# Kernel tuning notes

Measured on AMD Instinct MI355X. Metric: run time of the kernel, lower is better.

## Reference

```python
import jax, jax.numpy as jnp
import numpy as np

N_NODES = 50000
EPS = 1e-16


def seg_softmax(att, seg, n):
    # att: [E, H], softmax over edges sharing the same destination (seg)
    m = jax.ops.segment_max(att, seg, num_segments=n)
    m = jnp.where(jnp.isfinite(m), m, 0.0)
    e = jnp.exp(att - m[seg])
    s = jax.ops.segment_sum(e, seg, num_segments=n)
    return e / (s[seg] + EPS)


def gat_layer(x, W, b, a_l, a_r, row, col, n, nhead, out_feats, alpha, act):
    h = (x @ W).reshape(-1, nhead, out_feats)           # [N, H, F]
    h = jnp.nan_to_num(h)
    h_l = jnp.sum(a_l * h, axis=-1)                     # [N, H]
    h_r = jnp.sum(a_r * h, axis=-1)                     # [N, H]
    e = h_l[row] + h_r[col]                             # [E, H]
    e = jax.nn.leaky_relu(e, negative_slope=alpha)
    att = seg_softmax(e, row, n)                        # softmax per destination node
    # sparse multi-head aggregation: out[i] = sum_{e: row[e]=i} att[e] * h[col[e]]
    msg = att[:, :, None] * h[col]                      # [E, H, F]
    out = jax.ops.segment_sum(msg, row, num_segments=n) # [N, H, F]
    out = out.reshape(n, nhead * out_feats) + b
    if act:
        out = jax.nn.relu(out)
    return out


def setup_inputs() -> dict:
    key = jax.random.key(0)
    ks = jax.random.split(key, 10)
    N, E = N_NODES, 800000
    x = jax.random.normal(ks[0], (N, 256), dtype=jnp.float32)
    row = jax.random.randint(ks[1], (E,), 0, N)
    col = jax.random.randint(ks[2], (E,), 0, N)
    g = 1.414  # xavier-like scale handled via normal * small std
    W1 = jax.random.normal(ks[3], (256, 128), dtype=jnp.float32) * (g / np.sqrt(256 + 128))
    b1 = jnp.zeros((128,), dtype=jnp.float32)
    al1 = jax.random.normal(ks[4], (1, 4, 32), dtype=jnp.float32) * 0.1
    ar1 = jax.random.normal(ks[5], (1, 4, 32), dtype=jnp.float32) * 0.1
    W2 = jax.random.normal(ks[6], (128, 64), dtype=jnp.float32) * (g / np.sqrt(128 + 64))
    b2 = jnp.zeros((64,), dtype=jnp.float32)
    al2 = jax.random.normal(ks[7], (1, 1, 64), dtype=jnp.float32) * 0.1
    ar2 = jax.random.normal(ks[8], (1, 1, 64), dtype=jnp.float32) * 0.1
    return {"x": x, "row": row, "col": col, "W1": W1, "b1": b1, "al1": al1,
            "ar1": ar1, "W2": W2, "b2": b2, "al2": al2, "ar2": ar2}


def reference(x, row, col, W1, b1, al1, ar1, W2, b2, al2, ar2):
    n = N_NODES
    h = gat_layer(x, W1, b1, al1, ar1, row, col, n, nhead=4, out_feats=32, alpha=0.2, act=True)
    out = gat_layer(h, W2, b2, al2, ar2, row, col, n, nhead=1, out_feats=64, alpha=0.2, act=False)
    return out
```

## Files before the change

kernel.cpp:

```cpp
#include <hip/hip_runtime.h>
#include <hip/hip_bf16.h>
#include <hip/hip_fp16.h>
#include <math.h>

#define ALPHA 0.2f
#define LOG2E 1.44269504088896f
#define CAP 8192

typedef _Float16 half8 __attribute__((ext_vector_type(8)));
typedef float f32x4 __attribute__((ext_vector_type(4)));
typedef float f32x2 __attribute__((ext_vector_type(2)));

__global__ __launch_bounds__(256) void setup_kernel(
    int* __restrict__ gcursor,
    const float* __restrict__ W1, _Float16* __restrict__ W1t,
    const float* __restrict__ W2, _Float16* __restrict__ W2t) {
    const int blk = blockIdx.x, tid = threadIdx.x;
    if (blk == 0) {
        gcursor[tid] = 0;
    } else if (blk <= 128) {
        int i = (blk - 1) * 256 + tid;
        int k = i >> 7, c = i & 127;
        W1t[c * 256 + k] = (_Float16)W1[i];
    } else {
        int j = (blk - 129) * 256 + tid;
        int k = j >> 6, c = j & 63;
        W2t[c * 128 + k] = (_Float16)W2[j];
    }
}


__device__ __forceinline__ void part_body(char* smem, int blk,
                                          const int* __restrict__ row,
                                          const int* __restrict__ col,
                                          int* __restrict__ gcursor,
                                          unsigned* __restrict__ tmp, int E) {
    int* h = (int*)smem;
    int* rsv = h + 256;
    const int tid = threadIdx.x;
    const int base = blk * 4096;
    h[tid] = 0;
    __syncthreads();
#pragma unroll
    for (int k = 0; k < 16; ++k) {
        int i = base + k * 256 + tid;
        if (i < E) atomicAdd(&h[row[i] >> 8], 1);
    }
    __syncthreads();
    if (h[tid]) rsv[tid] = atomicAdd(&gcursor[tid], h[tid]);
    __syncthreads();
    h[tid] = 0;
    __syncthreads();
#pragma unroll
    for (int k = 0; k < 16; ++k) {
        int i = base + k * 256 + tid;
        if (i < E) {
            int r = row[i];
            int b = r >> 8;
            int loc = atomicAdd(&h[b], 1);
            tmp[(size_t)b * CAP + rsv[b] + loc] = ((unsigned)r << 16) | (unsigned)col[i];
        }
    }
}

__device__ __forceinline__ void bucket_body(char* smem, int k,
                                            const unsigned* __restrict__ tmp,
                                            const int* __restrict__ gcursor,
                                            unsigned* __restrict__ startcnt,
                                            unsigned short* __restrict__ csr_col, int N) {
    int* h = (int*)smem;
    int* rs = h + 256;
    int* wtot = rs + 256;
    const int tid = threadIdx.x;
    const int lane = tid & 63, wid = tid >> 6;
    const int base = k * CAP;
    const int count = gcursor[k];
    h[tid] = 0;
    __syncthreads();
    for (int p = tid; p < count; p += 256) atomicAdd(&h[(tmp[base + p] >> 16) & 255], 1);
    __syncthreads();
    int v = h[tid];
    int sc = v;
#pragma unroll
    for (int d = 1; d < 64; d <<= 1) {
        int u = __shfl_up(sc, d);
        if (lane >= d) sc += u;
    }
    if (lane == 63) wtot[wid] = sc;
    __syncthreads();
    int add = 0;
    for (int w = 0; w < wid; ++w) add += wtot[w];
    rs[tid] = sc - v + add + base;
    __syncthreads();
    int gr = k * 256 + tid;
    if (gr < N) startcnt[gr] = ((unsigned)rs[tid] << 11) | (unsigned)v;
    h[tid] = 0;
    __syncthreads();
    for (int p = tid; p < count; p += 256) {
        unsigned t = tmp[base + p];
        int rl = (t >> 16) & 255;
        int loc = atomicAdd(&h[rl], 1);
        csr_col[rs[rl] + loc] = (unsigned short)(t & 0xFFFF);
    }
}

__device__ __forceinline__ void gemm1_body(char* smem, int tile,
                                           const float* __restrict__ x,
                                           const _Float16* __restrict__ Wt,
                                           const float* __restrict__ al,
                                           const float* __restrict__ ar,
                                           unsigned char* __restrict__ h8,
                                           float* __restrict__ hl,
                                           float* __restrict__ hr, int N) {
    const int tid = threadIdx.x;
    const int lane = tid & 63, wc = tid >> 6;
    const int row0 = tile * 32;
    const int col0 = wc * 32;

#pragma unroll
    for (int it = 0; it < 8; ++it) {
        int i = it * 256 + tid;
        int r = i >> 6, c4 = i & 63;
        int gr = row0 + r;
        float4 v = {0.f, 0.f, 0.f, 0.f};
        if (gr < N) v = *(const float4*)(x + (size_t)gr * 256 + c4 * 4);
        union { _Float16 p[4]; uint2 u; } pk;
        pk.p[0] = (_Float16)v.x; pk.p[1] = (_Float16)v.y;
        pk.p[2] = (_Float16)v.z; pk.p[3] = (_Float16)v.w;
        int byte = r * 512 + c4 * 8;
        byte ^= (r & 7) << 4;
        *reinterpret_cast<uint2*>(smem + byte) = pk.u;
    }

    const _Float16* wbase = Wt + (size_t)(col0 + (lane & 15)) * 256 + (lane >> 4) * 8;

    __syncthreads();

    f32x4 acc[2][2] = {};
    half8 bf0[2], bf1[2], af0[2], af1[2];

    auto loadB = [&](int s, half8* dst) {
        dst[0] = *(const half8*)(wbase + s * 32);
        dst[1] = *(const half8*)(wbase + 16 * 256 + s * 32);
    };
    auto loadA = [&](int s, half8* dst) {
#pragma unroll
        for (int m = 0; m < 2; ++m) {
            int r = m * 16 + (lane & 15);
            int byte = r * 512 + s * 64 + (lane >> 4) * 16;
            byte ^= (r & 7) << 4;
            dst[m] = *reinterpret_cast<const half8*>(smem + byte);
        }
    };
    auto domfma = [&](half8* a, half8* bvec) {
#pragma unroll
        for (int m = 0; m < 2; ++m)
#pragma unroll
            for (int n = 0; n < 2; ++n)
                acc[m][n] = __builtin_amdgcn_mfma_f32_16x16x32_f16(
                    a[m], bvec[n], acc[m][n], 0, 0, 0);
    };

    loadB(0, bf0); loadA(0, af0);
#pragma unroll
    for (int s = 0; s < 8; s += 2) {
        if (s + 1 < 8) { loadB(s + 1, bf1); loadA(s + 1, af1); }
        domfma(af0, bf0);
        if (s + 2 < 8) { loadB(s + 2, bf0); loadA(s + 2, af0); }
        if (s + 1 < 8) domfma(af1, bf1);
    }

#pragma unroll
    for (int m = 0; m < 2; ++m) {
        int grow_base = row0 + m * 16 + (lane >> 4) * 4;
#pragma unroll
        for (int n = 0; n < 2; ++n) {
            int gcol = col0 + n * 16 + (lane & 15);
#pragma unroll
            for (int reg = 0; reg < 4; ++reg) {
                int grow = grow_base + reg;
                if (grow < N) {
                    unsigned pkv = __builtin_amdgcn_cvt_pk_fp8_f32(
                        acc[m][n][reg], acc[m][n][reg], 0, false);
                    h8[(size_t)grow * 128 + gcol] = (unsigned char)(pkv & 0xFF);
                }
            }
        }
    }

    const float al0 = al[col0 + (lane & 15)],      ar0 = ar[col0 + (lane & 15)];
    const float al1 = al[col0 + 16 + (lane & 15)], ar1 = ar[col0 + 16 + (lane & 15)];
#pragma unroll
    for (int m = 0; m < 2; ++m) {
#pragma unroll
        for (int reg = 0; reg < 4; ++reg) {
            float l = al0 * acc[m][0][reg] + al1 * acc[m][1][reg];
            float r = ar0 * acc[m][0][reg] + ar1 * acc[m][1][reg];
#pragma unroll
            for (int msk = 1; msk < 16; msk <<= 1) {
                l += __shfl_xor(l, msk);
                r += __shfl_xor(r, msk);
            }
            int grow = row0 + m * 16 + (lane >> 4) * 4 + reg;
            if ((lane & 15) == 0 && grow < N) {
                hl[grow * 4 + wc] = l * LOG2E;
                hr[grow * 4 + wc] = r * LOG2E;
            }
        }
    }
}

__global__ __launch_bounds__(256) void ka_kernel(
    const int* __restrict__ row, const int* __restrict__ col,
    int* __restrict__ gcursor, unsigned* __restrict__ tmp, int E, int eblocks,
    const float* __restrict__ x, const _Float16* __restrict__ W1t,
    const float* __restrict__ al, const float* __restrict__ ar,
    unsigned char* __restrict__ h8, float* __restrict__ hl, float* __restrict__ hr,
    int N, int tile0)
{
    __shared__ __align__(16) char smem[16384];
    if (blockIdx.x < (unsigned)eblocks)
        part_body(smem, blockIdx.x, row, col, gcursor, tmp, E);
    else
        gemm1_body(smem, tile0 + blockIdx.x - eblocks, x, W1t, al, ar, h8, hl, hr, N);
}

__global__ __launch_bounds__(256) void kb_kernel(
    const unsigned* __restrict__ tmp, const int* __restrict__ gcursor,
    unsigned* __restrict__ startcnt, unsigned short* __restrict__ csr_col,
    int nbuck,
    const float* __restrict__ x, const _Float16* __restrict__ W1t,
    const float* __restrict__ al, const float* __restrict__ ar,
    unsigned char* __restrict__ h8, float* __restrict__ hl, float* __restrict__ hr,
    int N, int tile0)
{
    __shared__ __align__(16) char smem[16384];
    if (blockIdx.x < (unsigned)nbuck)
        bucket_body(smem, blockIdx.x, tmp, gcursor, startcnt, csr_col, N);
    else
        gemm1_body(smem, tile0 + blockIdx.x - nbuck, x, W1t, al, ar, h8, hl, hr, N);
}

__global__ __launch_bounds__(256) void agg1g2_kernel(
    const unsigned* __restrict__ startcnt, const unsigned short* __restrict__ csr_col,
    const float* __restrict__ hls, const float* __restrict__ hrs,
    const unsigned char* __restrict__ h8, const float* __restrict__ b,
    const _Float16* __restrict__ W2t,
    const float* __restrict__ al, const float* __restrict__ ar,
    _Float16* __restrict__ h2, float* __restrict__ hl2, float* __restrict__ hr2, int N)
{
    __shared__ __align__(16) char rows[16 * 256];
    __shared__ float plds[16][4], prds[16][4];
    const int tid = threadIdx.x;
    const int lane = tid & 63, wid = tid >> 6;
    const int node0 = blockIdx.x * 16;
    const int q = lane >> 4;
    const int fl = lane & 15;
    const int head = fl >> 2;

    float bp[8];
#pragma unroll
    for (int k = 0; k < 8; ++k) bp[k] = b[8 * fl + k];

    for (int j = 0; j < 4; ++j) {
        const int i = node0 + wid * 4 + j;
        const int r = wid * 4 + j;
        float acc[8] = {};
        float den = 0.f;
        bool live = i < N;
        if (live) {
            const unsigned pk = startcnt[i];
            const int s = (int)(pk >> 11), e = s + (int)(pk & 2047);
            const float hlv = hls[i * 4 + head];

            int p0 = s + q;
            bool v0 = p0 < e;
            int cc0 = v0 ? (int)csr_col[p0] : 0;
            float hr0 = hrs[cc0 * 4 + head];
            uint2 g0 = *(const uint2*)(h8 + (size_t)cc0 * 128 + 8 * fl);

#pragma unroll 2
            for (int pb = s; pb < e; pb += 4) {
                int p1 = pb + 4 + q;
                bool v1 = p1 < e;
                int cc1 = v1 ? (int)csr_col[p1] : 0;
                float hr1v = hrs[cc1 * 4 + head];
                uint2 g1 = *(const uint2*)(h8 + (size_t)cc1 * 128 + 8 * fl);

                float sc = hlv + hr0;
                sc = sc > 0.f ? sc : ALPHA * sc;
                float w = exp2f(sc);
                w = v0 ? w : 0.f;
                den += w;
                f32x2 p01 = __builtin_amdgcn_cvt_pk_f32_fp8(g0.x, false);
                f32x2 p23 = __builtin_amdgcn_cvt_pk_f32_fp8(g0.x, true);
                f32x2 p45 = __builtin_amdgcn_cvt_pk_f32_fp8(g0.y, false);
                f32x2 p67 = __builtin_amdgcn_cvt_pk_f32_fp8(g0.y, true);
                acc[0] = fmaf(w, p01[0], acc[0]);
                acc[1] = fmaf(w, p01[1], acc[1]);
                acc[2] = fmaf(w, p23[0], acc[2]);
                acc[3] = fmaf(w, p23[1], acc[3]);
                acc[4] = fmaf(w, p45[0], acc[4]);
                acc[5] = fmaf(w, p45[1], acc[5]);
                acc[6] = fmaf(w, p67[0], acc[6]);
                acc[7] = fmaf(w, p67[1], acc[7]);

                v0 = v1; cc0 = cc1; hr0 = hr1v; g0 = g1;
            }

            den += __shfl_xor(den, 16); den += __shfl_xor(den, 32);
#pragma unroll
            for (int k = 0; k < 8; ++k) {
                acc[k] += __shfl_xor(acc[k], 16);
                acc[k] += __shfl_xor(acc[k], 32);
            }
        }
        if (lane < 16) {
            union { uint4 u; _Float16 q8[8]; } ov;
            if (live) {
                float rcp = 1.f / (den + 1e-16f);
#pragma unroll
                for (int k = 0; k < 8; ++k) {
                    float o = acc[k] * rcp + bp[k];
                    o = o > 0.f ? o : 0.f;
                    ov.q8[k] = (_Float16)o;
                }
            } else {
                ov.u = make_uint4(0, 0, 0, 0);
            }
            int byte = r * 256 + fl * 16;
            byte ^= (r & 7) << 4;
            *reinterpret_cast<uint4*>(rows + byte) = ov.u;
        }
    }
    __syncthreads();

    const int wc = wid;
    const int col0 = wc * 16;
    const _Float16* wbase = W2t + (size_t)(col0 + (lane & 15)) * 128 + (lane >> 4) * 8;

    f32x4 acc2 = {};
    half8 bf0, bf1, af0, af1;

    auto loadA = [&](int s, half8& dst) {
        int r = lane & 15;
        int byte = r * 256 + s * 64 + (lane >> 4) * 16;
        byte ^= (r & 7) << 4;
        dst = *reinterpret_cast<const half8*>(rows + byte);
    };

    bf0 = *(const half8*)(wbase); loadA(0, af0);
#pragma unroll
    for (int s = 0; s < 4; s += 2) {
        if (s + 1 < 4) { bf1 = *(const half8*)(wbase + (s + 1) * 32); loadA(s + 1, af1); }
        acc2 = __builtin_amdgcn_mfma_f32_16x16x32_f16(af0, bf0, acc2, 0, 0, 0);
        if (s + 2 < 4) { bf0 = *(const half8*)(wbase + (s + 2) * 32); loadA(s + 2, af0); }
        if (s + 1 < 4)
            acc2 = __builtin_amdgcn_mfma_f32_16x16x32_f16(af1, bf1, acc2, 0, 0, 0);
    }

    {
        int grow_base = node0 + (lane >> 4) * 4;
        int gcol = col0 + (lane & 15);
#pragma unroll
        for (int reg = 0; reg < 4; ++reg) {
            int grow = grow_base + reg;
            if (grow < N) h2[(size_t)grow * 64 + gcol] = (_Float16)acc2[reg];
        }
    }

    const float alv = al[col0 + (lane & 15)], arv = ar[col0 + (lane & 15)];
#pragma unroll
    for (int reg = 0; reg < 4; ++reg) {
        float l = alv * acc2[reg];
        float r = arv * acc2[reg];
#pragma unroll
        for (int msk = 1; msk < 16; msk <<= 1) {
            l += __shfl_xor(l, msk);
            r += __shfl_xor(r, msk);
        }
        int ri = (lane >> 4) * 4 + reg;
        if ((lane & 15) == 0) { plds[ri][wc] = l; prds[ri][wc] = r; }
    }
    __syncthreads();
    if (tid < 16) {
        int grow = node0 + tid;
        if (grow < N) {
            float l = plds[tid][0] + plds[tid][1] + plds[tid][2] + plds[tid][3];
            float r = prds[tid][0] + prds[tid][1] + prds[tid][2] + prds[tid][3];
            hl2[grow] = l * LOG2E;
            hr2[grow] = r * LOG2E;
        }
    }
}

__global__ __launch_bounds__(256) void agg2_kernel(
    const unsigned* __restrict__ startcnt, const unsigned short* __restrict__ csr_col,
    const float* __restrict__ hls, const float* __restrict__ hrs,
    const _Float16* __restrict__ h, const float* __restrict__ b,
    float* __restrict__ out, int N)
{
    const int i = blockIdx.x * 4 + (threadIdx.x >> 6);
    if (i >= N) return;
    const int lane = threadIdx.x & 63;
    const int q = lane >> 3;
    const int fl = lane & 7;
    const unsigned pk = startcnt[i];
    const int s = (int)(pk >> 11), e = s + (int)(pk & 2047);
    const float hlv = hls[i];

    float acc[8] = {};
    float den = 0.f;

    int p0 = s + q;
    bool v0 = p0 < e;
    int cc0 = v0 ? (int)csr_col[p0] : 0;
    float hr0 = hrs[cc0];
    uint4 g0 = *(const uint4*)(h + (size_t)cc0 * 64 + 8 * fl);

#pragma unroll 2
    for (int pb = s; pb < e; pb += 8) {
        int p1 = pb + 8 + q;
        bool v1 = p1 < e;
        int cc1 = v1 ? (int)csr_col[p1] : 0;
        float hr1v = hrs[cc1];
        uint4 g1 = *(const uint4*)(h + (size_t)cc1 * 64 + 8 * fl);

        float sc = hlv + hr0;
        sc = sc > 0.f ? sc : ALPHA * sc;
        float w = exp2f(sc);
        w = v0 ? w : 0.f;
        den += w;
        union { uint4 u; _Float16 q8[8]; } hv; hv.u = g0;
#pragma unroll
        for (int k = 0; k < 8; ++k) acc[k] = fmaf(w, (float)hv.q8[k], acc[k]);

        v0 = v1; cc0 = cc1; hr0 = hr1v; g0 = g1;
    }

    den += __shfl_xor(den, 8); den += __shfl_xor(den, 16); den += __shfl_xor(den, 32);
#pragma unroll
    for (int k = 0; k < 8; ++k) {
        acc[k] += __shfl_xor(acc[k], 8);
        acc[k] += __shfl_xor(acc[k], 16);
        acc[k] += __shfl_xor(acc[k], 32);
    }

    if (lane < 8) {
        float r = 1.f / (den + 1e-16f);
        const float* bp = b + 8 * fl;
        float4 o0, o1;
        o0.x = acc[0] * r + bp[0];
        o0.y = acc[1] * r + bp[1];
        o0.z = acc[2] * r + bp[2];
        o0.w = acc[3] * r + bp[3];
        o1.x = acc[4] * r + bp[4];
        o1.y = acc[5] * r + bp[5];
        o1.z = acc[6] * r + bp[6];
        o1.w = acc[7] * r + bp[7];
        float* op = out + (size_t)i * 64 + 8 * fl;
        *reinterpret_cast<float4*>(op) = o0;
        *reinterpret_cast<float4*>(op + 4) = o1;
    }
}

extern "C" void kernel_launch(void* const* d_in, const int* in_sizes, int n_in,
                              void* d_out, int out_size, void* d_ws, size_t ws_size,
                              hipStream_t stream)
{
    const float* x   = (const float*)d_in[0];
    const int*   row = (const int*)d_in[1];
    const int*   col = (const int*)d_in[2];
    const float* W1  = (const float*)d_in[3];
    const float* b1  = (const float*)d_in[4];
    const float* al1 = (const float*)d_in[5];
    const float* ar1 = (const float*)d_in[6];
    const float* W2  = (const float*)d_in[7];
    const float* b2  = (const float*)d_in[8];
    const float* al2 = (const float*)d_in[9];
    const float* ar2 = (const float*)d_in[10];
    const int N = in_sizes[0] / 256;
    const int E = in_sizes[1];
    const int nbuck = (N + 255) >> 8;
    float* out = (float*)d_out;

    size_t off_b = 0;
    auto alloc = [&](size_t bytes) -> void* {
        void* p = (char*)d_ws + off_b;
        off_b += (bytes + 255) & ~(size_t)255;
        return p;
    };
    int*            gcursor  = (int*)alloc((size_t)256 * 4);
    unsigned*       startcnt = (unsigned*)alloc((size_t)N * 4);
    unsigned*       tmp      = (unsigned*)alloc((size_t)nbuck * CAP * 4);
    unsigned short* csr_col  = (unsigned short*)alloc((size_t)nbuck * CAP * 2 + 32);
    _Float16*       W1t      = (_Float16*)alloc((size_t)128 * 256 * 2);
    _Float16*       W2t      = (_Float16*)alloc((size_t)64 * 128 * 2);
    unsigned char*  h1       = (unsigned char*)alloc((size_t)N * 128);
    float*          hl1      = (float*)alloc((size_t)N * 4 * 4);
    float*          hr1      = (float*)alloc((size_t)N * 4 * 4);
    _Float16*       h2       = (_Float16*)alloc((size_t)N * 64 * 2);
    float*          hl2      = (float*)alloc((size_t)N * 4);
    float*          hr2      = (float*)alloc((size_t)N * 4);
    (void)ws_size; (void)n_in; (void)out_size;

    const int eblocks = (E + 4095) / 4096;
    const int tiles = (N + 31) / 32;
    const int tilesA = (tiles + 1) / 2;
    const int tilesB = tiles - tilesA;

    setup_kernel<<<161, 256, 0, stream>>>(gcursor, W1, W1t, W2, W2t);
    ka_kernel<<<eblocks + tilesA, 256, 0, stream>>>(row, col, gcursor, tmp, E, eblocks,
                                                    x, W1t, al1, ar1, h1, hl1, hr1, N, 0);
    kb_kernel<<<nbuck + tilesB, 256, 0, stream>>>(tmp, gcursor, startcnt, csr_col, nbuck,
                                                  x, W1t, al1, ar1, h1, hl1, hr1, N, tilesA);

    agg1g2_kernel<<<(N + 15) / 16, 256, 0, stream>>>(startcnt, csr_col, hl1, hr1, h1, b1,
                                                     W2t, al2, ar2, h2, hl2, hr2, N);

    agg2_kernel<<<(N + 3) / 4, 256, 0, stream>>>(startcnt, csr_col, hl2, hr2, h2, b2, out, N);
}
```

Before: 109.4 us.

## Split layer-2 features into two column halves and aggregate each in separate passes

```diff
diff --git a/kernel.cpp b/kernel.cpp
--- a/kernel.cpp
+++ b/kernel.cpp
@@ -247,7 +247,8 @@
     const unsigned char* __restrict__ h8, const float* __restrict__ b,
     const _Float16* __restrict__ W2t,
     const float* __restrict__ al, const float* __restrict__ ar,
-    _Float16* __restrict__ h2, float* __restrict__ hl2, float* __restrict__ hr2, int N)
+    _Float16* __restrict__ h2a, _Float16* __restrict__ h2b,
+    float* __restrict__ hl2, float* __restrict__ hr2, int N)
 {
     __shared__ __align__(16) char rows[16 * 256];
     __shared__ float plds[16][4], prds[16][4];
@@ -362,10 +363,12 @@
     {
         int grow_base = node0 + (lane >> 4) * 4;
         int gcol = col0 + (lane & 15);
+        _Float16* hdst = (gcol < 32) ? h2a : h2b;
+        int hcol = gcol & 31;
 #pragma unroll
         for (int reg = 0; reg < 4; ++reg) {
             int grow = grow_base + reg;
-            if (grow < N) h2[(size_t)grow * 64 + gcol] = (_Float16)acc2[reg];
+            if (grow < N) hdst[(size_t)grow * 32 + hcol] = (_Float16)acc2[reg];
         }
     }
 
@@ -397,26 +400,29 @@
 __global__ __launch_bounds__(256) void agg2_kernel(
     const unsigned* __restrict__ startcnt, const unsigned short* __restrict__ csr_col,
     const float* __restrict__ hls, const float* __restrict__ hrs,
-    const _Float16* __restrict__ h, const float* __restrict__ b,
-    float* __restrict__ out, int N)
+    const _Float16* __restrict__ h2a, const _Float16* __restrict__ h2b,
+    const float* __restrict__ b, float* __restrict__ out, int N, int nodeblocks)
 {
-    const int i = blockIdx.x * 4 + (threadIdx.x >> 6);
+    const int sl = blockIdx.x / nodeblocks;
+    const int nb = blockIdx.x - sl * nodeblocks;
+    const int i = nb * 4 + (threadIdx.x >> 6);
     if (i >= N) return;
     const int lane = threadIdx.x & 63;
     const int q = lane >> 3;
     const int fl = lane & 7;
+    const _Float16* h = sl ? h2b : h2a;
     const unsigned pk = startcnt[i];
     const int s = (int)(pk >> 11), e = s + (int)(pk & 2047);
     const float hlv = hls[i];
 
-    float acc[8] = {};
+    float acc[4] = {};
     float den = 0.f;
 
     int p0 = s + q;
     bool v0 = p0 < e;
     int cc0 = v0 ? (int)csr_col[p0] : 0;
     float hr0 = hrs[cc0];
-    uint4 g0 = *(const uint4*)(h + (size_t)cc0 * 64 + 8 * fl);
+    uint2 g0 = *(const uint2*)(h + (size_t)cc0 * 32 + 4 * fl);
 
 #pragma unroll 2
     for (int pb = s; pb < e; pb += 8) {
@@ -424,23 +430,23 @@
         bool v1 = p1 < e;
         int cc1 = v1 ? (int)csr_col[p1] : 0;
         float hr1v = hrs[cc1];
-        uint4 g1 = *(const uint4*)(h + (size_t)cc1 * 64 + 8 * fl);
+        uint2 g1 = *(const uint2*)(h + (size_t)cc1 * 32 + 4 * fl);
 
         float sc = hlv + hr0;
         sc = sc > 0.f ? sc : ALPHA * sc;
         float w = exp2f(sc);
         w = v0 ? w : 0.f;
         den += w;
-        union { uint4 u; _Float16 q8[8]; } hv; hv.u = g0;
-#pragma unroll
-        for (int k = 0; k < 8; ++k) acc[k] = fmaf(w, (float)hv.q8[k], acc[k]);
+        union { uint2 u; _Float16 q4[4]; } hv; hv.u = g0;
+#pragma unroll
+        for (int k = 0; k < 4; ++k) acc[k] = fmaf(w, (float)hv.q4[k], acc[k]);
 
         v0 = v1; cc0 = cc1; hr0 = hr1v; g0 = g1;
     }
 
     den += __shfl_xor(den, 8); den += __shfl_xor(den, 16); den += __shfl_xor(den, 32);
 #pragma unroll
-    for (int k = 0; k < 8; ++k) {
+    for (int k = 0; k < 4; ++k) {
         acc[k] += __shfl_xor(acc[k], 8);
         acc[k] += __shfl_xor(acc[k], 16);
         acc[k] += __shfl_xor(acc[k], 32);
@@ -448,19 +454,13 @@
 
     if (lane < 8) {
         float r = 1.f / (den + 1e-16f);
-        const float* bp = b + 8 * fl;
-        float4 o0, o1;
-        o0.x = acc[0] * r + bp[0];
-        o0.y = acc[1] * r + bp[1];
-        o0.z = acc[2] * r + bp[2];
-        o0.w = acc[3] * r + bp[3];
-        o1.x = acc[4] * r + bp[4];
-        o1.y = acc[5] * r + bp[5];
-        o1.z = acc[6] * r + bp[6];
-        o1.w = acc[7] * r + bp[7];
-        float* op = out + (size_t)i * 64 + 8 * fl;
-        *reinterpret_cast<float4*>(op) = o0;
-        *reinterpret_cast<float4*>(op + 4) = o1;
+        const float* bp = b + sl * 32 + 4 * fl;
+        float4 ov;
+        ov.x = acc[0] * r + bp[0];
+        ov.y = acc[1] * r + bp[1];
+        ov.z = acc[2] * r + bp[2];
+        ov.w = acc[3] * r + bp[3];
+        *reinterpret_cast<float4*>(out + (size_t)i * 64 + sl * 32 + 4 * fl) = ov;
     }
 }
 
@@ -499,7 +499,8 @@
     unsigned char*  h1       = (unsigned char*)alloc((size_t)N * 128);
     float*          hl1      = (float*)alloc((size_t)N * 4 * 4);
     float*          hr1      = (float*)alloc((size_t)N * 4 * 4);
-    _Float16*       h2       = (_Float16*)alloc((size_t)N * 64 * 2);
+    _Float16*       h2a      = (_Float16*)alloc((size_t)N * 32 * 2);
+    _Float16*       h2b      = (_Float16*)alloc((size_t)N * 32 * 2);
     float*          hl2      = (float*)alloc((size_t)N * 4);
     float*          hr2      = (float*)alloc((size_t)N * 4);
     (void)ws_size; (void)n_in; (void)out_size;
@@ -508,6 +509,7 @@
     const int tiles = (N + 31) / 32;
     const int tilesA = (tiles + 1) / 2;
     const int tilesB = tiles - tilesA;
+    const int nodeblocks = (N + 3) / 4;
 
     setup_kernel<<<161, 256, 0, stream>>>(gcursor, W1, W1t, W2, W2t);
     ka_kernel<<<eblocks + tilesA, 256, 0, stream>>>(row, col, gcursor, tmp, E, eblocks,
@@ -516,7 +518,8 @@
                                                   x, W1t, al1, ar1, h1, hl1, hr1, N, tilesA);
 
     agg1g2_kernel<<<(N + 15) / 16, 256, 0, stream>>>(startcnt, csr_col, hl1, hr1, h1, b1,
-                                                     W2t, al2, ar2, h2, hl2, hr2, N);
-
-    agg2_kernel<<<(N + 3) / 4, 256, 0, stream>>>(startcnt, csr_col, hl2, hr2, h2, b2, out, N);
-}
+                                                     W2t, al2, ar2, h2a, h2b, hl2, hr2, N);
+
+    agg2_kernel<<<nodeblocks * 2, 256, 0, stream>>>(startcnt, csr_col, hl2, hr2,
+                                                    h2a, h2b, b2, out, N, nodeblocks);
+}
```

Result: slower. 123.4 us (+12.8%).
